# Optimization experiments

Hardware: AMD Instinct MI355X
Metric: run time of the kernel (lower is better)

The kernel has to match this reference:

```python
import jax, jax.numpy as jnp
import numpy as np

N, E, B = 50000, 600000, 64


def setup_inputs() -> dict:
    key = jax.random.key(0)
    ks = jax.random.split(key, 24)
    gn = lambda k, shape, s=0.1: jax.random.normal(k, shape, dtype=jnp.float32) * s
    return {
        "x": gn(ks[0], (N, 1), 1.0),
        "edge_index": jax.random.randint(ks[1], (2, E), 0, N),
        "batch": jnp.sort(jax.random.randint(ks[2], (N,), 0, B)),
        # GATConv(1,128)
        "W1": gn(ks[3], (1, 128)), "a1s": gn(ks[4], (128,)), "a1d": gn(ks[5], (128,)), "b1": jnp.zeros((128,), jnp.float32),
        # GATConv(128,128) x2
        "W2": gn(ks[6], (128, 128)), "a2s": gn(ks[7], (128,)), "a2d": gn(ks[8], (128,)), "b2": jnp.zeros((128,), jnp.float32),
        "W3": gn(ks[9], (128, 128)), "a3s": gn(ks[10], (128,)), "a3d": gn(ks[11], (128,)), "b3": jnp.zeros((128,), jnp.float32),
        # GCNConv(128,64), GCNConv(64,32)
        "Wg1": gn(ks[12], (128, 64)), "bg1": jnp.zeros((64,), jnp.float32),
        "Wg2": gn(ks[13], (64, 32)), "bg2": jnp.zeros((32,), jnp.float32),
        # SoftmaxAggregation learnable temperature (init 1.0)
        "t": jnp.ones((), jnp.float32),
        # Linear heads
        "Wl1": gn(ks[14], (32, 16)), "bl1": jnp.zeros((16,), jnp.float32),
        "Wl2": gn(ks[15], (16, 2)), "bl2": jnp.zeros((2,), jnp.float32),
    }


def reference(x, edge_index, batch, W1, a1s, a1d, b1, W2, a2s, a2d, b2,
              W3, a3s, a3d, b3, Wg1, bg1, Wg2, bg2, t, Wl1, bl1, Wl2, bl2):
    # add self-loops (PyG default for GATConv and GCNConv)
    loops = jnp.arange(N)
    ei = jnp.concatenate([edge_index, jnp.stack([loops, loops])], axis=1)
    src, dst = ei[0], ei[1]  # messages flow src -> dst

    def seg_softmax(logits, seg, num):
        m = jax.ops.segment_max(logits, seg, num)
        m = jnp.where(jnp.isfinite(m), m, 0.0)
        e = jnp.exp(logits - m[seg])
        s = jax.ops.segment_sum(e, seg, num)
        return e / (s[seg] + 1e-16)

    def gat(h_in, W, a_src, a_dst, b):
        h = h_in @ W                                   # [N, F]
        logit = jax.nn.leaky_relu((h @ a_src)[src] + (h @ a_dst)[dst], 0.2)
        alpha = seg_softmax(logit, dst, N)             # edge-softmax over neighbors of dst
        return jax.ops.segment_sum(alpha[:, None] * h[src], dst, N) + b

    def gcn(h_in, W, b):
        deg = jax.ops.segment_sum(jnp.ones(src.shape[0], h_in.dtype), dst, N)
        dinv = jnp.where(deg > 0, jax.lax.rsqrt(deg), 0.0)
        norm = dinv[src] * dinv[dst]                   # symmetric normalization
        h = h_in @ W
        return jax.ops.segment_sum(norm[:, None] * h[src], dst, N) + b

    h = jax.nn.elu(gat(x, W1, a1s, a1d, b1))
    h = jax.nn.elu(gat(h, W2, a2s, a2d, b2))
    h = jax.nn.elu(gat(h, W3, a3s, a3d, b3))
    h = jax.nn.elu(gcn(h, Wg1, bg1))
    h = jax.nn.elu(gcn(h, Wg2, bg2))

    # SoftmaxAggregation: per-graph, per-channel softmax weights w = softmax(t*h)
    logits = h * t
    m = jax.ops.segment_max(logits, batch, B)
    m = jnp.where(jnp.isfinite(m), m, 0.0)
    e = jnp.exp(logits - m[batch])
    s = jax.ops.segment_sum(e, batch, B)
    w = e / (s[batch] + 1e-16)
    g = jax.ops.segment_sum(w * h, batch, B)           # [B, 32]

    g = jax.nn.elu(g @ Wl1 + bl1)
    return jax.nn.log_softmax(g @ Wl2 + bl2, axis=1)
```

## Files before the change

### kernel.cpp

```cpp
#include <hip/hip_runtime.h>
#include <math.h>

static inline int cdiv(long a, long b){ return (int)((a + b - 1) / b); }
static inline char* alignp(char* p, size_t a){ return (char*)(((uintptr_t)p + a - 1) & ~(uintptr_t)(a - 1)); }

typedef __attribute__((ext_vector_type(8))) short bf16x8;
typedef __attribute__((ext_vector_type(4))) short bf16x4;
typedef __attribute__((ext_vector_type(4))) float f32x4;

__device__ __forceinline__ float lrelu(float x){ return x > 0.f ? x : 0.2f * x; }
__device__ __forceinline__ float eluf(float x){ return x > 0.f ? x : __expf(x) - 1.f; }
__device__ __forceinline__ short f2bf(float f){
  unsigned u = __float_as_uint(f);
  return (short)((u + 0x7FFFu + ((u >> 16) & 1u)) >> 16);
}
__device__ __forceinline__ float bflo(unsigned v){ return __uint_as_float(v << 16); }
__device__ __forceinline__ float bfhi(unsigned v){ return __uint_as_float(v & 0xFFFF0000u); }

template<int K, int FOUT, bool DOTS>
__global__ void k_gemm_mfma(const short* __restrict__ Abf, const short* __restrict__ Wp,
                            short* __restrict__ outb,
                            const float* __restrict__ av_s, const float* __restrict__ av_d,
                            float* __restrict__ as_, float* __restrict__ ad_, int N){
  constexpr int NKS = K / 32, NCT = FOUT / 16;
  int wid  = threadIdx.x >> 6;
  int lane = threadIdx.x & 63;
  int rowbase = (blockIdx.x * 4 + wid) * 16;
  if(rowbase >= N) return;
  int arow = rowbase + (lane & 15);
  if(arow >= N) arow = N - 1;
  f32x4 acc[NCT] = {};
  const short* ap = Abf + (long)arow * K + (lane >> 4) * 8;
  #pragma unroll
  for(int ks = 0; ks < NKS; ++ks){
    bf16x8 a = *(const bf16x8*)(ap + ks * 32);
    #pragma unroll
    for(int ct = 0; ct < NCT; ++ct){
      bf16x8 b = *(const bf16x8*)(Wp + ((ks * NCT + ct) * 64 + lane) * 8);
      acc[ct] = __builtin_amdgcn_mfma_f32_16x16x32_bf16(a, b, acc[ct], 0, 0, 0);
    }
  }
  int r0 = rowbase + (lane >> 4) * 4;
  int c0 = lane & 15;
  #pragma unroll
  for(int j = 0; j < 4; ++j){
    int r = r0 + j;
    if(r < N){
      #pragma unroll
      for(int ct = 0; ct < NCT; ++ct)
        outb[(long)r * FOUT + ct * 16 + c0] = f2bf(acc[ct][j]);
    }
  }
  if(DOTS){
    float avs[NCT], avd[NCT];
    #pragma unroll
    for(int ct = 0; ct < NCT; ++ct){ avs[ct] = av_s[ct * 16 + c0]; avd[ct] = av_d[ct * 16 + c0]; }
    #pragma unroll
    for(int j = 0; j < 4; ++j){
      float ps = 0.f, pd = 0.f;
      #pragma unroll
      for(int ct = 0; ct < NCT; ++ct){
        float hv = acc[ct][j];
        ps = fmaf(hv, avs[ct], ps);
        pd = fmaf(hv, avd[ct], pd);
      }
      #pragma unroll
      for(int off = 1; off < 16; off <<= 1){
        ps += __shfl_xor(ps, off);
        pd += __shfl_xor(pd, off);
      }
      int r = r0 + j;
      if(c0 == 0 && r < N){ as_[r] = ps; ad_[r] = pd; }
    }
  }
}

template<int K, int FOUT>
__global__ void k_pack_w(const float* __restrict__ W, short* __restrict__ Wp){
  constexpr int NKS = K / 32, NCT = FOUT / 16;
  int idx = blockIdx.x * blockDim.x + threadIdx.x;
  if(idx >= NKS * NCT * 64) return;
  int lane = idx & 63;
  int ct = (idx >> 6) % NCT;
  int ks = (idx >> 6) / NCT;
  int col = ct * 16 + (lane & 15);
  int kb  = ks * 32 + (lane >> 4) * 8;
  #pragma unroll
  for(int j = 0; j < 8; ++j) Wp[idx * 8 + j] = f2bf(W[(kb + j) * FOUT + col]);
}

__global__ void k_dot128(const float* __restrict__ W1, const float* __restrict__ a1s,
                         const float* __restrict__ a1d, float* __restrict__ S){
  __shared__ float s1[128], s2[128];
  int t = threadIdx.x;
  float w = W1[t];
  s1[t] = w * a1s[t]; s2[t] = w * a1d[t];
  __syncthreads();
  for(int off = 64; off > 0; off >>= 1){
    if(t < off){ s1[t] += s1[t + off]; s2[t] += s2[t + off]; }
    __syncthreads();
  }
  if(t == 0){ S[0] = s1[0]; S[1] = s2[0]; }
}
__global__ void k_l1v(const float* __restrict__ x, const float* __restrict__ W1,
                      short* __restrict__ outb, int N){
  long idx = (long)blockIdx.x * blockDim.x + threadIdx.x;
  if(idx >= (long)N * 16) return;
  int node = (int)(idx >> 4), j8 = ((int)idx & 15) * 8;
  float xv = x[node];
  float4 w0 = *(const float4*)(W1 + j8);
  float4 w1 = *(const float4*)(W1 + j8 + 4);
  bf16x8 v;
  v[0] = f2bf(xv * w0.x); v[1] = f2bf(xv * w0.y);
  v[2] = f2bf(xv * w0.z); v[3] = f2bf(xv * w0.w);
  v[4] = f2bf(xv * w1.x); v[5] = f2bf(xv * w1.y);
  v[6] = f2bf(xv * w1.z); v[7] = f2bf(xv * w1.w);
  *(bf16x8*)(outb + (long)node * 128 + j8) = v;
}
__global__ void k_l1dots(const float* __restrict__ x, const float* __restrict__ S,
                         float* __restrict__ as_, float* __restrict__ ad_, int N){
  int i = blockIdx.x * blockDim.x + threadIdx.x;
  if(i >= N) return;
  float xv = x[i];
  as_[i] = xv * S[0]; ad_[i] = xv * S[1];
}

__global__ void k_deg_init(int* __restrict__ deg, int N){
  int i = blockIdx.x * blockDim.x + threadIdx.x;
  if(i < N) deg[i] = 1;
}
__global__ void k_deg_count(const int* __restrict__ ei, int E, int* __restrict__ deg){
  int e = blockIdx.x * blockDim.x + threadIdx.x;
  if(e < E) atomicAdd(&deg[ei[E + e]], 1);
}

__global__ void k_scan_part(const int* __restrict__ deg, int* __restrict__ bsum, int N){
  __shared__ int red[256];
  int i = blockIdx.x * 256 + threadIdx.x;
  int v = (i < N) ? deg[i] : 0;
  red[threadIdx.x] = v;
  __syncthreads();
  #pragma unroll
  for(int off = 128; off > 0; off >>= 1){
    if(threadIdx.x < off) red[threadIdx.x] += red[threadIdx.x + off];
    __syncthreads();
  }
  if(threadIdx.x == 0) bsum[blockIdx.x] = red[0];
}
__global__ void k_scan_mid(int* __restrict__ bsum, int NB, int* __restrict__ rowptr, int N){
  __shared__ int buf[1024];
  int t = threadIdx.x;
  int v = (t < NB) ? bsum[t] : 0;
  buf[t] = v;
  __syncthreads();
  for(int off = 1; off < 1024; off <<= 1){
    int u = (t >= off) ? buf[t - off] : 0;
    __syncthreads();
    buf[t] += u;
    __syncthreads();
  }
  if(t < NB) bsum[t] = buf[t] - v;
  if(t == 1023) rowptr[N] = buf[1023];
}
__global__ void k_scan_fin(const int* __restrict__ deg, const int* __restrict__ bsum,
                           int* __restrict__ rowptr, int* __restrict__ cursor, int N){
  __shared__ int buf[256];
  int i = blockIdx.x * 256 + threadIdx.x;
  int t = threadIdx.x;
  int v = (i < N) ? deg[i] : 0;
  buf[t] = v;
  __syncthreads();
  #pragma unroll
  for(int off = 1; off < 256; off <<= 1){
    int u = (t >= off) ? buf[t - off] : 0;
    __syncthreads();
    buf[t] += u;
    __syncthreads();
  }
  if(i < N){
    int ex = buf[t] - v + bsum[blockIdx.x];
    rowptr[i] = ex; cursor[i] = ex;
  }
}

__global__ void k_fill(const int* __restrict__ ei, int E, int N,
                       int* __restrict__ cursor, int* __restrict__ csr_src){
  int e = blockIdx.x * blockDim.x + threadIdx.x;
  if(e >= E + N) return;
  int s, d;
  if(e < E){ s = ei[e]; d = ei[E + e]; } else { s = e - E; d = s; }
  int pos = atomicAdd(&cursor[d], 1);
  csr_src[pos] = s;
}
__global__ void k_dinv(const int* __restrict__ deg, float* __restrict__ dinv, int N){
  int i = blockIdx.x * blockDim.x + threadIdx.x;
  if(i < N) dinv[i] = rsqrtf((float)deg[i]);
}

__global__ void k_gat_agg(const int* __restrict__ rowptr, const int* __restrict__ csr,
                          const float* __restrict__ as_, const float* __restrict__ ad_,
                          const short* __restrict__ h, const float* __restrict__ bias,
                          short* __restrict__ out, int N){
  int w = (int)(((long)blockIdx.x * blockDim.x + threadIdx.x) >> 6);
  int lane = threadIdx.x & 63;
  if(w >= N) return;
  int start = rowptr[w], end = rowptr[w + 1];
  int deg = end - start;
  float add = ad_[w];

  int s_reg = 0;
  float alpha_reg = 0.f, m, inv;
  if(deg <= 64){
    float logit = -INFINITY;
    if(lane < deg){
      s_reg = csr[start + lane];
      logit = lrelu(as_[s_reg] + add);
    }
    m = logit;
    #pragma unroll
    for(int off = 32; off > 0; off >>= 1) m = fmaxf(m, __shfl_xor(m, off));
    float e = __expf(logit - m);
    float ssum = e;
    #pragma unroll
    for(int off = 32; off > 0; off >>= 1) ssum += __shfl_xor(ssum, off);
    inv = 1.f / (ssum + 1e-16f);
    alpha_reg = e * inv;
  }else{
    float logit = -INFINITY, ssum = 0.f;
    m = -INFINITY;
    if(lane < deg){
      s_reg = csr[start + lane];
      logit = lrelu(as_[s_reg] + add);
      m = logit; ssum = 1.f;
      for(int e = start + lane + 64; e < end; e += 64){
        int s = csr[e];
        float l = lrelu(as_[s] + add);
        if(l > m){ ssum = ssum * __expf(m - l) + 1.f; m = l; }
        else       ssum += __expf(l - m);
      }
    }
    #pragma unroll
    for(int off = 32; off > 0; off >>= 1){
      float mo = __shfl_xor(m, off);
      float so = __shfl_xor(ssum, off);
      float mn = fmaxf(m, mo);
      float ea = (m  > -INFINITY) ? __expf(m  - mn) : 0.f;
      float eb = (mo > -INFINITY) ? __expf(mo - mn) : 0.f;
      ssum = ssum * ea + so * eb;
      m = mn;
    }
    inv = 1.f / (ssum + 1e-16f);
    alpha_reg = __expf(logit - m) * inv;
  }

  float acc[8] = {};
  int nb = deg < 64 ? deg : 64;
  int g  = lane >> 4;
  int fo = (lane & 15) * 8;
  const short* hf = h + fo;
  for(int k = 0; k < nb; k += 4){
    int idx = k + g;
    if(idx < nb){
      float a = __shfl(alpha_reg, idx);
      int s   = __shfl(s_reg, idx);
      uint4 hv = *(const uint4*)(hf + (long)s * 128);
      acc[0] = fmaf(a, bflo(hv.x), acc[0]);
      acc[1] = fmaf(a, bfhi(hv.x), acc[1]);
      acc[2] = fmaf(a, bflo(hv.y), acc[2]);
      acc[3] = fmaf(a, bfhi(hv.y), acc[3]);
      acc[4] = fmaf(a, bflo(hv.z), acc[4]);
      acc[5] = fmaf(a, bfhi(hv.z), acc[5]);
      acc[6] = fmaf(a, bflo(hv.w), acc[6]);
      acc[7] = fmaf(a, bfhi(hv.w), acc[7]);
    }
  }
  for(int e = start + 64; e < end; ++e){
    if(lane < 16){
      int s = csr[e];
      float l = lrelu(as_[s] + add);
      float a = __expf(l - m) * inv;
      uint4 hv = *(const uint4*)(hf + (long)s * 128);
      acc[0] = fmaf(a, bflo(hv.x), acc[0]);
      acc[1] = fmaf(a, bfhi(hv.x), acc[1]);
      acc[2] = fmaf(a, bflo(hv.y), acc[2]);
      acc[3] = fmaf(a, bfhi(hv.y), acc[3]);
      acc[4] = fmaf(a, bflo(hv.z), acc[4]);
      acc[5] = fmaf(a, bfhi(hv.z), acc[5]);
      acc[6] = fmaf(a, bflo(hv.w), acc[6]);
      acc[7] = fmaf(a, bfhi(hv.w), acc[7]);
    }
  }
  #pragma unroll
  for(int j = 0; j < 8; ++j){
    acc[j] += __shfl_xor(acc[j], 16);
    acc[j] += __shfl_xor(acc[j], 32);
  }
  if(lane < 16){
    float4 b0 = *(const float4*)(bias + fo);
    float4 b1 = *(const float4*)(bias + fo + 4);
    bf16x8 v;
    v[0] = f2bf(eluf(acc[0] + b0.x)); v[1] = f2bf(eluf(acc[1] + b0.y));
    v[2] = f2bf(eluf(acc[2] + b0.z)); v[3] = f2bf(eluf(acc[3] + b0.w));
    v[4] = f2bf(eluf(acc[4] + b1.x)); v[5] = f2bf(eluf(acc[5] + b1.y));
    v[6] = f2bf(eluf(acc[6] + b1.z)); v[7] = f2bf(eluf(acc[7] + b1.w));
    *(bf16x8*)(out + (long)w * 128 + fo) = v;
  }
}

template<int F, bool BFOUT>
__global__ void k_gcn_agg(const int* __restrict__ rowptr, const int* __restrict__ csr,
                          const float* __restrict__ dinv, const short* __restrict__ h,
                          const float* __restrict__ bias, short* __restrict__ out_bf,
                          float* __restrict__ out_f, int N){
  constexpr int FPL = F / 16;
  int w = (int)(((long)blockIdx.x * blockDim.x + threadIdx.x) >> 6);
  int lane = threadIdx.x & 63;
  if(w >= N) return;
  int start = rowptr[w], end = rowptr[w + 1];
  int deg = end - start;
  float dd = dinv[w];
  int s_reg = 0; float dv_reg = 0.f;
  if(lane < deg){
    s_reg = csr[start + lane];
    dv_reg = dinv[s_reg];
  }
  float acc[FPL] = {};
  int nb = deg < 64 ? deg : 64;
  int g  = lane >> 4;
  int fo = (lane & 15) * FPL;
  const short* hf = h + fo;
  for(int k = 0; k < nb; k += 4){
    int idx = k + g;
    if(idx < nb){
      int s = __shfl(s_reg, idx);
      float nrm = dd * __shfl(dv_reg, idx);
      if(FPL == 4){
        uint2 hv = *(const uint2*)(hf + (long)s * F);
        acc[0] = fmaf(nrm, bflo(hv.x), acc[0]);
        acc[1] = fmaf(nrm, bfhi(hv.x), acc[1]);
        acc[2] = fmaf(nrm, bflo(hv.y), acc[2]);
        acc[3] = fmaf(nrm, bfhi(hv.y), acc[3]);
      }else{
        unsigned hv = *(const unsigned*)(hf + (long)s * F);
        acc[0] = fmaf(nrm, bflo(hv), acc[0]);
        acc[1] = fmaf(nrm, bfhi(hv), acc[1]);
      }
    }
  }
  for(int e = start + 64; e < end; ++e){
    if(lane < 16){
      int s = csr[e];
      float nrm = dd * dinv[s];
      if(FPL == 4){
        uint2 hv = *(const uint2*)(hf + (long)s * F);
        acc[0] = fmaf(nrm, bflo(hv.x), acc[0]);
        acc[1] = fmaf(nrm, bfhi(hv.x), acc[1]);
        acc[2] = fmaf(nrm, bflo(hv.y), acc[2]);
        acc[3] = fmaf(nrm, bfhi(hv.y), acc[3]);
      }else{
        unsigned hv = *(const unsigned*)(hf + (long)s * F);
        acc[0] = fmaf(nrm, bflo(hv), acc[0]);
        acc[1] = fmaf(nrm, bfhi(hv), acc[1]);
      }
    }
  }
  #pragma unroll
  for(int j = 0; j < FPL; ++j){
    acc[j] += __shfl_xor(acc[j], 16);
    acc[j] += __shfl_xor(acc[j], 32);
  }
  if(lane < 16){
    if(BFOUT){
      if(FPL == 4){
        bf16x4 v;
        #pragma unroll
        for(int j = 0; j < 4; ++j) v[j] = f2bf(eluf(acc[j] + bias[fo + j]));
        *(bf16x4*)(out_bf + (long)w * F + fo) = v;
      }else{
        #pragma unroll
        for(int j = 0; j < FPL; ++j)
          out_bf[(long)w * F + fo + j] = f2bf(eluf(acc[j] + bias[fo + j]));
      }
    }else{
      if(FPL == 2){
        float2 v2 = make_float2(eluf(acc[0] + bias[fo]), eluf(acc[1] + bias[fo + 1]));
        *(float2*)(out_f + (long)w * F + fo) = v2;
      }else{
        #pragma unroll
        for(int j = 0; j < FPL; ++j)
          out_f[(long)w * F + fo + j] = eluf(acc[j] + bias[fo + j]);
      }
    }
  }
}

template<int S>
__global__ void k_bagg_part(const float* __restrict__ h, const int* __restrict__ batch,
                            const float* __restrict__ t, float* __restrict__ pM,
                            float* __restrict__ pS, float* __restrict__ pV, int N){
  int chunk = blockIdx.x;
  int b = chunk / S, s = chunk % S;
  __shared__ int s_lo, s_hi;
  if(threadIdx.x == 0){
    int lo = 0, hi = N;
    while(lo < hi){ int mid = (lo + hi) >> 1; if(batch[mid] < b) lo = mid + 1; else hi = mid; }
    s_lo = lo;
    int lo2 = lo, hi2 = N;
    while(lo2 < hi2){ int mid = (lo2 + hi2) >> 1; if(batch[mid] < b + 1) lo2 = mid + 1; else hi2 = mid; }
    s_hi = lo2;
  }
  __syncthreads();
  int lo = s_lo, hi = s_hi;
  int len = hi - lo;
  int per = (len + S - 1) / S;
  int clo = lo + s * per;
  int chi = clo + per; if(chi > hi) chi = hi;
  float tv = t[0];
  int c = threadIdx.x & 31, r = threadIdx.x >> 5;

  float m = -INFINITY, ss = 0.f, vv = 0.f;
  for(int i = clo + r; i < chi; i += 8){
    float hv = h[(long)i * 32 + c];
    float l = hv * tv;
    if(l > m){
      float e = (m > -INFINITY) ? __expf(m - l) : 0.f;
      ss = ss * e + 1.f; vv = vv * e + hv; m = l;
    }else{
      float e = __expf(l - m);
      ss += e; vv += e * hv;
    }
  }
  __shared__ float rm[8][32], rs[8][32], rv[8][32];
  rm[r][c] = m; rs[r][c] = ss; rv[r][c] = vv;
  __syncthreads();
  if(r == 0){
    float M = rm[0][c], SS = rs[0][c], VV = rv[0][c];
    #pragma unroll
    for(int k = 1; k < 8; ++k){
      float mo = rm[k][c], so = rs[k][c], vo = rv[k][c];
      float mn = fmaxf(M, mo);
      float ea = (M  > -INFINITY) ? __expf(M  - mn) : 0.f;
      float eb = (mo > -INFINITY) ? __expf(mo - mn) : 0.f;
      SS = SS * ea + so * eb; VV = VV * ea + vo * eb; M = mn;
    }
    pM[chunk * 32 + c] = M; pS[chunk * 32 + c] = SS; pV[chunk * 32 + c] = VV;
  }
}
template<int S>
__global__ void k_bagg_comb(const float* __restrict__ pM, const float* __restrict__ pS,
                            const float* __restrict__ pV, float* __restrict__ g, int B){
  int idx = blockIdx.x * blockDim.x + threadIdx.x;
  if(idx >= B * 32) return;
  int b = idx >> 5, c = idx & 31;
  float M = -INFINITY, SS = 0.f, VV = 0.f;
  #pragma unroll 4
  for(int k = 0; k < S; ++k){
    int p = (b * S + k) * 32 + c;
    float mo = pM[p], so = pS[p], vo = pV[p];
    float mn = fmaxf(M, mo);
    float ea = (M  > -INFINITY) ? __expf(M  - mn) : 0.f;
    float eb = (mo > -INFINITY) ? __expf(mo - mn) : 0.f;
    SS = SS * ea + so * eb; VV = VV * ea + vo * eb; M = mn;
  }
  g[idx] = VV / (SS + 1e-16f);
}

__global__ void k_head(const float* __restrict__ g, const float* __restrict__ Wl1,
                       const float* __restrict__ bl1, const float* __restrict__ Wl2,
                       const float* __restrict__ bl2, float* __restrict__ out, int B){
  int b = blockIdx.x * blockDim.x + threadIdx.x;
  if(b >= B) return;
  float gr[32];
  #pragma unroll
  for(int k = 0; k < 32; ++k) gr[k] = g[b * 32 + k];
  float h1[16];
  #pragma unroll
  for(int j = 0; j < 16; ++j){
    float acc = bl1[j];
    #pragma unroll
    for(int k = 0; k < 32; ++k) acc = fmaf(gr[k], Wl1[k * 16 + j], acc);
    h1[j] = eluf(acc);
  }
  float l0 = bl2[0], l1 = bl2[1];
  #pragma unroll
  for(int k = 0; k < 16; ++k){
    l0 = fmaf(h1[k], Wl2[k * 2 + 0], l0);
    l1 = fmaf(h1[k], Wl2[k * 2 + 1], l1);
  }
  float mx = fmaxf(l0, l1);
  float lse = mx + __logf(__expf(l0 - mx) + __expf(l1 - mx));
  out[b * 2 + 0] = l0 - lse;
  out[b * 2 + 1] = l1 - lse;
}

extern "C" void kernel_launch(void* const* d_in, const int* in_sizes, int n_in,
                              void* d_out, int out_size, void* d_ws, size_t ws_size,
                              hipStream_t stream){
  const float* x     = (const float*)d_in[0];
  const int*   ei    = (const int*)d_in[1];
  const int*   batch = (const int*)d_in[2];
  const float* W1 = (const float*)d_in[3];
  const float* a1s = (const float*)d_in[4];
  const float* a1d = (const float*)d_in[5];
  const float* b1 = (const float*)d_in[6];
  const float* W2 = (const float*)d_in[7];
  const float* a2s = (const float*)d_in[8];
  const float* a2d = (const float*)d_in[9];
  const float* b2 = (const float*)d_in[10];
  const float* W3 = (const float*)d_in[11];
  const float* a3s = (const float*)d_in[12];
  const float* a3d = (const float*)d_in[13];
  const float* b3 = (const float*)d_in[14];
  const float* Wg1 = (const float*)d_in[15];
  const float* bg1 = (const float*)d_in[16];
  const float* Wg2 = (const float*)d_in[17];
  const float* bg2 = (const float*)d_in[18];
  const float* t   = (const float*)d_in[19];
  const float* Wl1 = (const float*)d_in[20];
  const float* bl1 = (const float*)d_in[21];
  const float* Wl2 = (const float*)d_in[22];
  const float* bl2 = (const float*)d_in[23];

  const int N = in_sizes[0];
  const int E = in_sizes[1] / 2;
  const int B = out_size / 2;
  const int ET = E + N;
  float* out = (float*)d_out;
  constexpr int BS = 32;

  char* p = (char*)d_ws;
  short* Hbf  = (short*)p;            p += (size_t)N * 128 * 2;
  short* Abf  = (short*)p;            p += (size_t)N * 128 * 2;
  float* A32  = (float*)p;            p += (size_t)N * 32 * 4;
  float* as_  = (float*)p;            p += (size_t)N * 4;
  float* ad_  = (float*)p;            p += (size_t)N * 4;
  float* dinv = (float*)p;            p += (size_t)N * 4;
  int*   deg    = (int*)p;            p += (size_t)N * 4;
  int*   rowptr = (int*)p;            p += (size_t)(N + 1) * 4;
  int*   cursor = (int*)p;            p += (size_t)N * 4;
  int*   csr    = (int*)p;            p += (size_t)ET * 4;
  int*   bsum   = (int*)p;            p += (size_t)1024 * 4;
  p = alignp(p, 16);
  short* Wp2  = (short*)p;            p += 128 * 128 * 2;
  short* Wp3  = (short*)p;            p += 128 * 128 * 2;
  short* Wpg1 = (short*)p;            p += 128 * 64 * 2;
  short* Wpg2 = (short*)p;            p += 64 * 32 * 2;
  p = alignp(p, 16);
  float* S    = (float*)p;            p += 16 * 4;
  float* pM   = (float*)p;            p += (size_t)B * BS * 32 * 4;
  float* pSb  = (float*)p;            p += (size_t)B * BS * 32 * 4;
  float* pV   = (float*)p;            p += (size_t)B * BS * 32 * 4;
  float* g    = (float*)p;

  const int T = 256;
  const int gN  = cdiv(N, T);
  const int gE  = cdiv(E, T);
  const int gET = cdiv(ET, T);
  const int gW  = cdiv((long)N * 64, T);
  const int gG  = cdiv(N, 64);
  const int NB  = cdiv(N, 256);

  k_deg_init<<<dim3(gN), dim3(T), 0, stream>>>(deg, N);
  k_deg_count<<<dim3(gE), dim3(T), 0, stream>>>(ei, E, deg);
  k_scan_part<<<dim3(NB), dim3(256), 0, stream>>>(deg, bsum, N);
  k_scan_mid<<<dim3(1), dim3(1024), 0, stream>>>(bsum, NB, rowptr, N);
  k_scan_fin<<<dim3(NB), dim3(256), 0, stream>>>(deg, bsum, rowptr, cursor, N);
  k_fill<<<dim3(gET), dim3(T), 0, stream>>>(ei, E, N, cursor, csr);
  k_dinv<<<dim3(gN), dim3(T), 0, stream>>>(deg, dinv, N);
  k_pack_w<128,128><<<dim3(8), dim3(T), 0, stream>>>(W2, Wp2);
  k_pack_w<128,128><<<dim3(8), dim3(T), 0, stream>>>(W3, Wp3);
  k_pack_w<128, 64><<<dim3(4), dim3(T), 0, stream>>>(Wg1, Wpg1);
  k_pack_w< 64, 32><<<dim3(1), dim3(T), 0, stream>>>(Wg2, Wpg2);
  k_dot128<<<dim3(1), dim3(128), 0, stream>>>(W1, a1s, a1d, S);

  k_l1v<<<dim3(cdiv((long)N * 16, T)), dim3(T), 0, stream>>>(x, W1, Hbf, N);
  k_l1dots<<<dim3(gN), dim3(T), 0, stream>>>(x, S, as_, ad_, N);
  k_gat_agg<<<dim3(gW), dim3(T), 0, stream>>>(rowptr, csr, as_, ad_, Hbf, b1, Abf, N);

  k_gemm_mfma<128,128,true><<<dim3(gG), dim3(T), 0, stream>>>(Abf, Wp2, Hbf, a2s, a2d, as_, ad_, N);
  k_gat_agg<<<dim3(gW), dim3(T), 0, stream>>>(rowptr, csr, as_, ad_, Hbf, b2, Abf, N);

  k_gemm_mfma<128,128,true><<<dim3(gG), dim3(T), 0, stream>>>(Abf, Wp3, Hbf, a3s, a3d, as_, ad_, N);
  k_gat_agg<<<dim3(gW), dim3(T), 0, stream>>>(rowptr, csr, as_, ad_, Hbf, b3, Abf, N);

  k_gemm_mfma<128,64,false><<<dim3(gG), dim3(T), 0, stream>>>(Abf, Wpg1, Hbf, nullptr, nullptr, nullptr, nullptr, N);
  k_gcn_agg<64,true><<<dim3(gW), dim3(T), 0, stream>>>(rowptr, csr, dinv, Hbf, bg1, Abf, (float*)nullptr, N);

  k_gemm_mfma<64,32,false><<<dim3(gG), dim3(T), 0, stream>>>(Abf, Wpg2, Hbf, nullptr, nullptr, nullptr, nullptr, N);
  k_gcn_agg<32,false><<<dim3(gW), dim3(T), 0, stream>>>(rowptr, csr, dinv, Hbf, bg2, (short*)nullptr, A32, N);

  k_bagg_part<BS><<<dim3(B * BS), dim3(256), 0, stream>>>(A32, batch, t, pM, pSb, pV, N);
  k_bagg_comb<BS><<<dim3(cdiv(B * 32, 256)), dim3(256), 0, stream>>>(pM, pSb, pV, g, B);

  k_head<<<dim3(cdiv(B, 64)), dim3(64), 0, stream>>>(g, Wl1, bl1, Wl2, bl2, out, B);
}
```

Baseline: 315.4 us.

## Partition degree-count and CSR-fill atomics by destination range across XCDs

```diff
diff --git a/kernel.cpp b/kernel.cpp
--- a/kernel.cpp
+++ b/kernel.cpp
@@ -129,9 +129,15 @@
   int i = blockIdx.x * blockDim.x + threadIdx.x;
   if(i < N) deg[i] = 1;
 }
-__global__ void k_deg_count(const int* __restrict__ ei, int E, int* __restrict__ deg){
-  int e = blockIdx.x * blockDim.x + threadIdx.x;
-  if(e < E) atomicAdd(&deg[ei[E + e]], 1);
+__global__ void k_deg_count8(const int* __restrict__ ei, int E, int Pdiv,
+                             int* __restrict__ deg){
+  int p = blockIdx.x & 7;
+  int lo = p * Pdiv, hi = lo + Pdiv;
+  long stride = (long)(gridDim.x >> 3) * blockDim.x;
+  for(long e = (long)(blockIdx.x >> 3) * blockDim.x + threadIdx.x; e < E; e += stride){
+    int d = ei[E + e];
+    if(d >= lo && d < hi) atomicAdd(&deg[d], 1);
+  }
 }
 
 __global__ void k_scan_part(const int* __restrict__ deg, int* __restrict__ bsum, int N){
@@ -163,7 +169,8 @@
   if(t == 1023) rowptr[N] = buf[1023];
 }
 __global__ void k_scan_fin(const int* __restrict__ deg, const int* __restrict__ bsum,
-                           int* __restrict__ rowptr, int* __restrict__ cursor, int N){
+                           int* __restrict__ rowptr, int* __restrict__ cursor,
+                           float* __restrict__ dinv, int N){
   __shared__ int buf[256];
   int i = blockIdx.x * 256 + threadIdx.x;
   int t = threadIdx.x;
@@ -180,21 +187,23 @@
   if(i < N){
     int ex = buf[t] - v + bsum[blockIdx.x];
     rowptr[i] = ex; cursor[i] = ex;
-  }
-}
-
-__global__ void k_fill(const int* __restrict__ ei, int E, int N,
-                       int* __restrict__ cursor, int* __restrict__ csr_src){
-  int e = blockIdx.x * blockDim.x + threadIdx.x;
-  if(e >= E + N) return;
-  int s, d;
-  if(e < E){ s = ei[e]; d = ei[E + e]; } else { s = e - E; d = s; }
-  int pos = atomicAdd(&cursor[d], 1);
-  csr_src[pos] = s;
-}
-__global__ void k_dinv(const int* __restrict__ deg, float* __restrict__ dinv, int N){
-  int i = blockIdx.x * blockDim.x + threadIdx.x;
-  if(i < N) dinv[i] = rsqrtf((float)deg[i]);
+    dinv[i] = rsqrtf((float)v);
+  }
+}
+
+__global__ void k_fill8(const int* __restrict__ ei, int E, int N, int Pdiv,
+                        int* __restrict__ cursor, int* __restrict__ csr){
+  int p = blockIdx.x & 7;
+  int lo = p * Pdiv, hi = lo + Pdiv;
+  long ET = (long)E + N;
+  long stride = (long)(gridDim.x >> 3) * blockDim.x;
+  for(long e = (long)(blockIdx.x >> 3) * blockDim.x + threadIdx.x; e < ET; e += stride){
+    int d = (e < E) ? ei[E + e] : (int)(e - E);
+    if(d < lo || d >= hi) continue;
+    int s = (e < E) ? ei[e] : d;
+    int pos = atomicAdd(&cursor[d], 1);
+    csr[pos] = s;
+  }
 }
 
 __global__ void k_gat_agg(const int* __restrict__ rowptr, const int* __restrict__ csr,
@@ -554,19 +563,17 @@
 
   const int T = 256;
   const int gN  = cdiv(N, T);
-  const int gE  = cdiv(E, T);
-  const int gET = cdiv(ET, T);
   const int gW  = cdiv((long)N * 64, T);
   const int gG  = cdiv(N, 64);
   const int NB  = cdiv(N, 256);
+  const int Pdiv = cdiv(N, 8);
 
   k_deg_init<<<dim3(gN), dim3(T), 0, stream>>>(deg, N);
-  k_deg_count<<<dim3(gE), dim3(T), 0, stream>>>(ei, E, deg);
+  k_deg_count8<<<dim3(2048), dim3(T), 0, stream>>>(ei, E, Pdiv, deg);
   k_scan_part<<<dim3(NB), dim3(256), 0, stream>>>(deg, bsum, N);
   k_scan_mid<<<dim3(1), dim3(1024), 0, stream>>>(bsum, NB, rowptr, N);
-  k_scan_fin<<<dim3(NB), dim3(256), 0, stream>>>(deg, bsum, rowptr, cursor, N);
-  k_fill<<<dim3(gET), dim3(T), 0, stream>>>(ei, E, N, cursor, csr);
-  k_dinv<<<dim3(gN), dim3(T), 0, stream>>>(deg, dinv, N);
+  k_scan_fin<<<dim3(NB), dim3(256), 0, stream>>>(deg, bsum, rowptr, cursor, dinv, N);
+  k_fill8<<<dim3(2048), dim3(T), 0, stream>>>(ei, E, N, Pdiv, cursor, csr);
   k_pack_w<128,128><<<dim3(8), dim3(T), 0, stream>>>(W2, Wp2);
   k_pack_w<128,128><<<dim3(8), dim3(T), 0, stream>>>(W3, Wp3);
   k_pack_w<128, 64><<<dim3(4), dim3(T), 0, stream>>>(Wg1, Wpg1);
```

Result: faster. 307.5 us (-2.5%).
